# Kernel optimization log

Measured on AMD Instinct MI355X. Metric: run time of the kernel, lower is better.

The kernel has to match this reference:

```python
import jax, jax.numpy as jnp
import numpy as np

F_IN, N_TREES, DEPTH, TREE_DIM, BATCH = 256, 512, 6, 3, 512


def entmax15_axis0(z):
    """Exact 1.5-entmax along axis 0 (sort-based algorithm from Peters et al. 2019)."""
    z = z / 2.0
    z = z - jnp.max(z, axis=0, keepdims=True)
    zs = -jnp.sort(-z, axis=0)                      # descending sort, [F, N]
    F = z.shape[0]
    rho = jnp.arange(1, F + 1, dtype=z.dtype)[:, None]
    mean = jnp.cumsum(zs, axis=0) / rho
    mean_sq = jnp.cumsum(zs * zs, axis=0) / rho
    ss = rho * (mean_sq - mean * mean)
    delta = (1.0 - ss) / rho
    tau = mean - jnp.sqrt(jnp.clip(delta, 0.0))
    support = (tau <= zs).astype(jnp.int32)
    k = jnp.sum(support, axis=0) - 1                # last valid index per column
    tau_star = jnp.take_along_axis(tau, k[None, :], axis=0)
    return jnp.square(jnp.clip(z - tau_star, 0.0))


def setup_inputs() -> dict:
    key = jax.random.key(0)
    k0, k1, k2, k3 = jax.random.split(key, 4)
    return {
        "input": jax.random.normal(k0, (BATCH, F_IN), jnp.float32),
        "feat_attention": jax.random.uniform(k1, (F_IN, N_TREES * DEPTH), jnp.float32),
        "feature_thresholds": jax.random.normal(k2, (N_TREES, DEPTH), jnp.float32) * 0.1,
        "log_temperatures": jnp.zeros((N_TREES, DEPTH), jnp.float32),
        "response": jax.random.normal(k3, (N_TREES, TREE_DIM, 2 ** DEPTH), jnp.float32),
    }


def reference(input, feat_attention, feature_thresholds, log_temperatures, response):
    T, D = feature_thresholds.shape
    F = feat_attention.shape[0]
    # sparse feature selection per (tree, depth)
    choice_weight = entmax15_axis0(feat_attention).reshape(F, T, D)
    feature_values = jnp.einsum('bi,ind->bnd', input, choice_weight)      # [B, T, D]
    # thresholding with learned temperature, bin_func == '05_01'
    tl = (feature_values - feature_thresholds) * jnp.exp(-log_temperatures)
    tl = jnp.stack([-tl, tl], axis=-1)                                    # [B, T, D, 2]
    bins = jnp.clip(0.5 * tl + 0.5, -0.5, 1.5)
    # binary codes of the 2^D leaves: [D, 2^D, 2]
    idx = jnp.arange(2 ** D)
    off = 2 ** jnp.arange(D)
    bc = ((idx[None, :] // off[:, None]) % 2).astype(bins.dtype)
    codes = jnp.stack([bc, 1.0 - bc], axis=-1)
    # depth-wise outer product into leaf weights
    bin_matches = jnp.einsum('btds,dcs->btdc', bins, codes)               # [B, T, D, 2^D]
    response_weights = jnp.prod(bin_matches, axis=-2)                     # [B, T, 2^D]
    out = jnp.einsum('bnd,ncd->bnc', response_weights, response)          # [B, T, C]
    return out.reshape(out.shape[0], -1)
```

## Files before the change

### kernel.cpp

```cpp
#include <hip/hip_runtime.h>
#include <math.h>

#define F_IN 256
#define NTREES 512
#define DEPTH 6
#define NCOLS (NTREES * DEPTH)
#define BATCH 512
#define OUTW (NTREES * 3)

__global__ __launch_bounds__(256) void k_entmax(const float* __restrict__ att,
                                                float* __restrict__ cw) {
    const int n0 = blockIdx.x * 16;
    const int tid = threadIdx.x;
    const int lane = tid & 63;
    const int w = tid >> 6;
    __shared__ float s_z[16][260];

    const int cld = tid & 15;
#pragma unroll
    for (int it = 0; it < 16; ++it) {
        int f = (tid >> 4) + it * 16;
        s_z[cld][f] = att[f * NCOLS + n0 + cld];
    }
    __syncthreads();

    float4 z[4];
    float m[4], tau[4];
#pragma unroll
    for (int c = 0; c < 4; ++c) {
        float4 v = *(const float4*)&s_z[w * 4 + c][4 * lane];
        z[c] = make_float4(v.x * 0.5f, v.y * 0.5f, v.z * 0.5f, v.w * 0.5f);
        m[c] = fmaxf(fmaxf(z[c].x, z[c].y), fmaxf(z[c].z, z[c].w));
    }
#pragma unroll
    for (int off = 32; off >= 1; off >>= 1)
#pragma unroll
        for (int c = 0; c < 4; ++c)
            m[c] = fmaxf(m[c], __shfl_xor(m[c], off));
#pragma unroll
    for (int c = 0; c < 4; ++c) {
        z[c].x -= m[c]; z[c].y -= m[c]; z[c].z -= m[c]; z[c].w -= m[c];
        tau[c] = -1.0f;
    }

    for (int iter = 0; iter < 14; ++iter) {
        float S1[4], S2[4];
#pragma unroll
        for (int c = 0; c < 4; ++c) {
            float d0 = fmaxf(z[c].x - tau[c], 0.f);
            float d1 = fmaxf(z[c].y - tau[c], 0.f);
            float d2 = fmaxf(z[c].z - tau[c], 0.f);
            float d3 = fmaxf(z[c].w - tau[c], 0.f);
            S1[c] = (d0 + d1) + (d2 + d3);
            S2[c] = fmaf(d0, d0, fmaf(d1, d1, fmaf(d2, d2, d3 * d3)));
        }
#pragma unroll
        for (int off = 32; off >= 1; off >>= 1)
#pragma unroll
            for (int c = 0; c < 4; ++c) {
                S1[c] += __shfl_xor(S1[c], off);
                S2[c] += __shfl_xor(S2[c], off);
            }
        bool done = true;
#pragma unroll
        for (int c = 0; c < 4; ++c) {
            tau[c] += (S2[c] - 1.f) / (2.f * S1[c]);
            done = done && (fabsf(S2[c] - 1.f) < 4e-6f);
        }
        if (done) break;
    }

#pragma unroll
    for (int c = 0; c < 4; ++c) {
        float4 pv;
        float v0 = fmaxf(z[c].x - tau[c], 0.f);
        float v1 = fmaxf(z[c].y - tau[c], 0.f);
        float v2 = fmaxf(z[c].z - tau[c], 0.f);
        float v3 = fmaxf(z[c].w - tau[c], 0.f);
        pv.x = v0 * v0; pv.y = v1 * v1; pv.z = v2 * v2; pv.w = v3 * v3;
        *(float4*)&s_z[w * 4 + c][4 * lane] = pv;
    }
    __syncthreads();
#pragma unroll
    for (int it = 0; it < 16; ++it) {
        int f = (tid >> 4) + it * 16;
        cw[f * NCOLS + n0 + cld] = s_z[cld][f];
    }
}

__global__ __launch_bounds__(256) void k_gemm(const float* __restrict__ cw,
                                              const float* __restrict__ inp,
                                              float* __restrict__ fv) {
    const int n0 = blockIdx.x * 64;
    const int b0 = blockIdx.y * 64;
    const int tid = threadIdx.x;
    __shared__ float sA[16][64];
    __shared__ float sB[16][68];
    const int tx = tid & 15, ty = tid >> 4;
    const int a_k = tid >> 4, a_n = (tid & 15) * 4;
    const int b_b = tid >> 2, b_k = (tid & 3) * 4;
    float acc[4][4] = {};
    for (int f0 = 0; f0 < F_IN; f0 += 16) {
        float4 av = *(const float4*)&cw[(f0 + a_k) * NCOLS + n0 + a_n];
        float4 bv = *(const float4*)&inp[(b0 + b_b) * F_IN + f0 + b_k];
        __syncthreads();
        *(float4*)&sA[a_k][a_n] = av;
        sB[b_k + 0][b_b] = bv.x;
        sB[b_k + 1][b_b] = bv.y;
        sB[b_k + 2][b_b] = bv.z;
        sB[b_k + 3][b_b] = bv.w;
        __syncthreads();
#pragma unroll
        for (int kk = 0; kk < 16; ++kk) {
            float a[4], b[4];
#pragma unroll
            for (int i = 0; i < 4; ++i) a[i] = sA[kk][ty * 4 + i];
#pragma unroll
            for (int j = 0; j < 4; ++j) b[j] = sB[kk][tx * 4 + j];
#pragma unroll
            for (int i = 0; i < 4; ++i)
#pragma unroll
                for (int j = 0; j < 4; ++j)
                    acc[i][j] = fmaf(a[i], b[j], acc[i][j]);
        }
    }
#pragma unroll
    for (int i = 0; i < 4; ++i) {
        float4 v = make_float4(acc[i][0], acc[i][1], acc[i][2], acc[i][3]);
        *(float4*)&fv[(n0 + ty * 4 + i) * BATCH + b0 + tx * 4] = v;
    }
}

__global__ __launch_bounds__(256) void k_tree(const float* __restrict__ fv,
                                              const float* __restrict__ thr,
                                              const float* __restrict__ ltemp,
                                              const float* __restrict__ resp,
                                              float* __restrict__ out) {
    const int t0 = blockIdx.x * 8;
    const int b0 = blockIdx.y * 64;
    const int tid = threadIdx.x;
    const int bl = tid & 63;
    const int b = b0 + bl;
    const int tsub = tid >> 6;
    __shared__ float s_resp[8 * 192];
    __shared__ float s_out[64][25];

    for (int i = tid; i < 8 * 192; i += 256)
        s_resp[i] = resp[t0 * 192 + i];
    __syncthreads();

#pragma unroll
    for (int half_t = 0; half_t < 2; ++half_t) {
        const int ttl = tsub + half_t * 4;
        const int tt = t0 + ttl;
        float bpos[6], bneg[6];
#pragma unroll
        for (int d = 0; d < 6; ++d) {
            float fvv = fv[(tt * 6 + d) * BATCH + b];
            float tl = (fvv - thr[tt * 6 + d]) * expf(-ltemp[tt * 6 + d]);
            float hp = 0.5f * tl + 0.5f;
            float hn = 0.5f - 0.5f * tl;
            bpos[d] = fminf(fmaxf(hp, -0.5f), 1.5f);
            bneg[d] = fminf(fmaxf(hn, -0.5f), 1.5f);
        }
        float p[64];
        p[0] = 1.f;
#pragma unroll
        for (int d = 0; d < 6; ++d) {
            int half = 1 << d;
#pragma unroll 32
            for (int i = half - 1; i >= 0; --i) {
                float v = p[i];
                p[i + half] = v * bneg[d];
                p[i]        = v * bpos[d];
            }
        }
        float a0 = 0.f, a1 = 0.f, a2 = 0.f;
        const float* r = &s_resp[ttl * 192];
#pragma unroll
        for (int c = 0; c < 64; ++c) {
            a0 = fmaf(p[c], r[c], a0);
            a1 = fmaf(p[c], r[64 + c], a1);
            a2 = fmaf(p[c], r[128 + c], a2);
        }
        s_out[bl][ttl * 3 + 0] = a0;
        s_out[bl][ttl * 3 + 1] = a1;
        s_out[bl][ttl * 3 + 2] = a2;
    }
    __syncthreads();
    for (int i = tid; i < 64 * 24; i += 256) {
        int row = i / 24, col = i % 24;
        out[(b0 + row) * OUTW + t0 * 3 + col] = s_out[row][col];
    }
}

extern "C" void kernel_launch(void* const* d_in, const int* in_sizes, int n_in,
                              void* d_out, int out_size, void* d_ws, size_t ws_size,
                              hipStream_t stream) {
    const float* input = (const float*)d_in[0];
    const float* att   = (const float*)d_in[1];
    const float* thr   = (const float*)d_in[2];
    const float* ltemp = (const float*)d_in[3];
    const float* resp  = (const float*)d_in[4];
    float* out = (float*)d_out;

    float* cw = (float*)d_ws;
    float* fv = cw + F_IN * NCOLS;

    hipLaunchKernelGGL(k_entmax, dim3(NCOLS / 16), dim3(256), 0, stream, att, cw);
    hipLaunchKernelGGL(k_gemm, dim3(NCOLS / 64, BATCH / 64), dim3(256), 0, stream,
                       cw, input, fv);
    hipLaunchKernelGGL(k_tree, dim3(NTREES / 8, BATCH / 64), dim3(256), 0, stream,
                       fv, thr, ltemp, resp, out);
}
```

Baseline: 98.39 us.

## Fuse feature GEMM with tree evaluation and store choice weights transposed

The GEMM and tree-evaluation kernels become one kernel. Each block computes the 48 feature values for its 8 trees and 64 batch rows into shared memory, then evaluates the trees directly, so the fv intermediate no longer makes a round trip through global memory and one launch is dropped. The entmax kernel now writes the choice weights transposed (column-major over features) with float4 stores, and the GEMM uses a K-tile of 64 with a 3x4 register tile. The trade-offs are higher shared-memory use per block (about 47KB), which may lower occupancy, and a smaller per-thread register tile in the GEMM.

```diff
diff --git a/kernel.cpp b/kernel.cpp
--- a/kernel.cpp
+++ b/kernel.cpp
@@ -9,7 +9,7 @@
 #define OUTW (NTREES * 3)
 
 __global__ __launch_bounds__(256) void k_entmax(const float* __restrict__ att,
-                                                float* __restrict__ cw) {
+                                                float* __restrict__ cwT) {
     const int n0 = blockIdx.x * 16;
     const int tid = threadIdx.x;
     const int lane = tid & 63;
@@ -81,116 +81,134 @@
         *(float4*)&s_z[w * 4 + c][4 * lane] = pv;
     }
     __syncthreads();
-#pragma unroll
-    for (int it = 0; it < 16; ++it) {
-        int f = (tid >> 4) + it * 16;
-        cw[f * NCOLS + n0 + cld] = s_z[cld][f];
+    const int nl = tid >> 4;
+    const int f0 = (tid & 15) * 16;
+#pragma unroll
+    for (int j = 0; j < 4; ++j) {
+        float4 v = *(const float4*)&s_z[nl][f0 + 4 * j];
+        *(float4*)&cwT[(n0 + nl) * F_IN + f0 + 4 * j] = v;
     }
 }
 
-__global__ __launch_bounds__(256) void k_gemm(const float* __restrict__ cw,
-                                              const float* __restrict__ inp,
-                                              float* __restrict__ fv) {
-    const int n0 = blockIdx.x * 64;
-    const int b0 = blockIdx.y * 64;
+__global__ __launch_bounds__(256) void k_fused(const float* __restrict__ cwT,
+                                               const float* __restrict__ inp,
+                                               const float* __restrict__ thr,
+                                               const float* __restrict__ ltemp,
+                                               const float* __restrict__ resp,
+                                               float* __restrict__ out) {
+    const int tb  = blockIdx.x;
+    const int b0  = blockIdx.y * 64;
+    const int t0g = tb * 8;
+    const int n0g = tb * 48;
     const int tid = threadIdx.x;
-    __shared__ float sA[16][64];
-    __shared__ float sB[16][68];
-    const int tx = tid & 15, ty = tid >> 4;
-    const int a_k = tid >> 4, a_n = (tid & 15) * 4;
-    const int b_b = tid >> 2, b_k = (tid & 3) * 4;
-    float acc[4][4] = {};
-    for (int f0 = 0; f0 < F_IN; f0 += 16) {
-        float4 av = *(const float4*)&cw[(f0 + a_k) * NCOLS + n0 + a_n];
-        float4 bv = *(const float4*)&inp[(b0 + b_b) * F_IN + f0 + b_k];
+
+    __shared__ float sA[64][48];
+    __shared__ float sB[64][68];
+    __shared__ float sFV[48][68];
+    __shared__ float sR[8 * 192];
+    __shared__ float sO[64][25];
+
+    for (int i = tid; i < 8 * 192; i += 256) sR[i] = resp[t0g * 192 + i];
+
+    const int tx = tid & 15;
+    const int ty = tid >> 4;
+    const int a_w = tid >> 6;
+    const int a_k = tid & 63;
+    const int b_b = tid >> 2;
+    const int b_k = (tid & 3) * 16;
+    float acc[3][4] = {};
+
+    for (int k0 = 0; k0 < F_IN; k0 += 64) {
+        float a_reg[12];
+#pragma unroll
+        for (int i = 0; i < 12; ++i)
+            a_reg[i] = cwT[(n0g + i * 4 + a_w) * F_IN + k0 + a_k];
+        float4 b_reg[4];
+#pragma unroll
+        for (int i = 0; i < 4; ++i)
+            b_reg[i] = *(const float4*)&inp[(b0 + b_b) * F_IN + k0 + b_k + i * 4];
         __syncthreads();
-        *(float4*)&sA[a_k][a_n] = av;
-        sB[b_k + 0][b_b] = bv.x;
-        sB[b_k + 1][b_b] = bv.y;
-        sB[b_k + 2][b_b] = bv.z;
-        sB[b_k + 3][b_b] = bv.w;
+#pragma unroll
+        for (int i = 0; i < 12; ++i) sA[a_k][i * 4 + a_w] = a_reg[i];
+#pragma unroll
+        for (int i = 0; i < 4; ++i) {
+            sB[b_k + i * 4 + 0][b_b] = b_reg[i].x;
+            sB[b_k + i * 4 + 1][b_b] = b_reg[i].y;
+            sB[b_k + i * 4 + 2][b_b] = b_reg[i].z;
+            sB[b_k + i * 4 + 3][b_b] = b_reg[i].w;
+        }
         __syncthreads();
-#pragma unroll
-        for (int kk = 0; kk < 16; ++kk) {
-            float a[4], b[4];
-#pragma unroll
-            for (int i = 0; i < 4; ++i) a[i] = sA[kk][ty * 4 + i];
-#pragma unroll
-            for (int j = 0; j < 4; ++j) b[j] = sB[kk][tx * 4 + j];
-#pragma unroll
-            for (int i = 0; i < 4; ++i)
-#pragma unroll
-                for (int j = 0; j < 4; ++j)
-                    acc[i][j] = fmaf(a[i], b[j], acc[i][j]);
-        }
-    }
-#pragma unroll
-    for (int i = 0; i < 4; ++i) {
-        float4 v = make_float4(acc[i][0], acc[i][1], acc[i][2], acc[i][3]);
-        *(float4*)&fv[(n0 + ty * 4 + i) * BATCH + b0 + tx * 4] = v;
-    }
-}
-
-__global__ __launch_bounds__(256) void k_tree(const float* __restrict__ fv,
-                                              const float* __restrict__ thr,
-                                              const float* __restrict__ ltemp,
-                                              const float* __restrict__ resp,
-                                              float* __restrict__ out) {
-    const int t0 = blockIdx.x * 8;
-    const int b0 = blockIdx.y * 64;
-    const int tid = threadIdx.x;
-    const int bl = tid & 63;
-    const int b = b0 + bl;
-    const int tsub = tid >> 6;
-    __shared__ float s_resp[8 * 192];
-    __shared__ float s_out[64][25];
-
-    for (int i = tid; i < 8 * 192; i += 256)
-        s_resp[i] = resp[t0 * 192 + i];
-    __syncthreads();
-
-#pragma unroll
-    for (int half_t = 0; half_t < 2; ++half_t) {
-        const int ttl = tsub + half_t * 4;
-        const int tt = t0 + ttl;
+#pragma unroll 16
+        for (int kk = 0; kk < 64; ++kk) {
+            float a0 = sA[kk][ty * 3 + 0];
+            float a1 = sA[kk][ty * 3 + 1];
+            float a2 = sA[kk][ty * 3 + 2];
+            float4 bv = *(const float4*)&sB[kk][tx * 4];
+            acc[0][0] = fmaf(a0, bv.x, acc[0][0]);
+            acc[0][1] = fmaf(a0, bv.y, acc[0][1]);
+            acc[0][2] = fmaf(a0, bv.z, acc[0][2]);
+            acc[0][3] = fmaf(a0, bv.w, acc[0][3]);
+            acc[1][0] = fmaf(a1, bv.x, acc[1][0]);
+            acc[1][1] = fmaf(a1, bv.y, acc[1][1]);
+            acc[1][2] = fmaf(a1, bv.z, acc[1][2]);
+            acc[1][3] = fmaf(a1, bv.w, acc[1][3]);
+            acc[2][0] = fmaf(a2, bv.x, acc[2][0]);
+            acc[2][1] = fmaf(a2, bv.y, acc[2][1]);
+            acc[2][2] = fmaf(a2, bv.z, acc[2][2]);
+            acc[2][3] = fmaf(a2, bv.w, acc[2][3]);
+        }
+    }
+#pragma unroll
+    for (int r = 0; r < 3; ++r) {
+        float4 v = make_float4(acc[r][0], acc[r][1], acc[r][2], acc[r][3]);
+        *(float4*)&sFV[ty * 3 + r][tx * 4] = v;
+    }
+    __syncthreads();
+
+#pragma unroll
+    for (int p = 0; p < 2; ++p) {
+        const int pi = p * 256 + tid;
+        const int tl = pi >> 6;
+        const int b  = pi & 63;
+        const int base = (t0g + tl) * 6;
         float bpos[6], bneg[6];
 #pragma unroll
         for (int d = 0; d < 6; ++d) {
-            float fvv = fv[(tt * 6 + d) * BATCH + b];
-            float tl = (fvv - thr[tt * 6 + d]) * expf(-ltemp[tt * 6 + d]);
-            float hp = 0.5f * tl + 0.5f;
-            float hn = 0.5f - 0.5f * tl;
+            float fvv = sFV[tl * 6 + d][b];
+            float tlv = (fvv - thr[base + d]) * expf(-ltemp[base + d]);
+            float hp = 0.5f * tlv + 0.5f;
+            float hn = 0.5f - 0.5f * tlv;
             bpos[d] = fminf(fmaxf(hp, -0.5f), 1.5f);
             bneg[d] = fminf(fmaxf(hn, -0.5f), 1.5f);
         }
-        float p[64];
-        p[0] = 1.f;
+        float pr[64];
+        pr[0] = 1.f;
 #pragma unroll
         for (int d = 0; d < 6; ++d) {
             int half = 1 << d;
 #pragma unroll 32
             for (int i = half - 1; i >= 0; --i) {
-                float v = p[i];
-                p[i + half] = v * bneg[d];
-                p[i]        = v * bpos[d];
+                float v = pr[i];
+                pr[i + half] = v * bneg[d];
+                pr[i]        = v * bpos[d];
             }
         }
         float a0 = 0.f, a1 = 0.f, a2 = 0.f;
-        const float* r = &s_resp[ttl * 192];
+        const float* r = &sR[tl * 192];
 #pragma unroll
         for (int c = 0; c < 64; ++c) {
-            a0 = fmaf(p[c], r[c], a0);
-            a1 = fmaf(p[c], r[64 + c], a1);
-            a2 = fmaf(p[c], r[128 + c], a2);
-        }
-        s_out[bl][ttl * 3 + 0] = a0;
-        s_out[bl][ttl * 3 + 1] = a1;
-        s_out[bl][ttl * 3 + 2] = a2;
+            a0 = fmaf(pr[c], r[c], a0);
+            a1 = fmaf(pr[c], r[64 + c], a1);
+            a2 = fmaf(pr[c], r[128 + c], a2);
+        }
+        sO[b][tl * 3 + 0] = a0;
+        sO[b][tl * 3 + 1] = a1;
+        sO[b][tl * 3 + 2] = a2;
     }
     __syncthreads();
     for (int i = tid; i < 64 * 24; i += 256) {
         int row = i / 24, col = i % 24;
-        out[(b0 + row) * OUTW + t0 * 3 + col] = s_out[row][col];
+        out[(b0 + row) * OUTW + t0g * 3 + col] = sO[row][col];
     }
 }
 
@@ -204,12 +222,9 @@
     const float* resp  = (const float*)d_in[4];
     float* out = (float*)d_out;
 
-    float* cw = (float*)d_ws;
-    float* fv = cw + F_IN * NCOLS;
-
-    hipLaunchKernelGGL(k_entmax, dim3(NCOLS / 16), dim3(256), 0, stream, att, cw);
-    hipLaunchKernelGGL(k_gemm, dim3(NCOLS / 64, BATCH / 64), dim3(256), 0, stream,
-                       cw, input, fv);
-    hipLaunchKernelGGL(k_tree, dim3(NTREES / 8, BATCH / 64), dim3(256), 0, stream,
-                       fv, thr, ltemp, resp, out);
+    float* cwT = (float*)d_ws;
+
+    hipLaunchKernelGGL(k_entmax, dim3(NCOLS / 16), dim3(256), 0, stream, att, cwT);
+    hipLaunchKernelGGL(k_fused, dim3(NTREES / 8, BATCH / 64), dim3(256), 0, stream,
+                       cwT, input, thr, ltemp, resp, out);
 }
```

Result: slower. 101.3 us (+2.9%).

## Run feature GEMM on bf16 MFMA with hi/lo split for fp32 accuracy

Applied to the files above, without the earlier changes.

The fp32 SIMT GEMM is replaced by a matrix-core kernel that uses bf16 16x16x32 MFMA. Each operand is split into bf16 high and low parts, and three products (hh, hl, lh) are accumulated to approximate fp32 precision. The entmax kernel now writes the choice weights transposed and pre-split. Extra blocks in the same launch split the input matrix, so the GEMM reads K-contiguous operands straight from global memory with no LDS. The cost is three times the MFMA work and extra workspace traffic for the split arrays, plus a small accuracy risk from the dropped lo*lo term.

```diff
diff --git a/kernel.cpp b/kernel.cpp
--- a/kernel.cpp
+++ b/kernel.cpp
@@ -8,10 +8,48 @@
 #define BATCH 512
 #define OUTW (NTREES * 3)
 
+typedef __attribute__((ext_vector_type(8))) short bf16x8;
+typedef __attribute__((ext_vector_type(4))) float f32x4;
+typedef __attribute__((ext_vector_type(4))) unsigned short u16x4;
+typedef __attribute__((ext_vector_type(8))) unsigned short u16x8;
+
+__device__ __forceinline__ unsigned short f2bf(float x) {
+    unsigned u = __float_as_uint(x);
+    return (unsigned short)((u + 0x7FFFu + ((u >> 16) & 1u)) >> 16);
+}
+__device__ __forceinline__ void split2(float x, unsigned short& h, unsigned short& l) {
+    h = f2bf(x);
+    l = f2bf(x - __uint_as_float((unsigned)h << 16));
+}
+
 __global__ __launch_bounds__(256) void k_entmax(const float* __restrict__ att,
-                                                float* __restrict__ cw) {
+                                                const float* __restrict__ inp,
+                                                unsigned short* __restrict__ cwT_hi,
+                                                unsigned short* __restrict__ cwT_lo,
+                                                unsigned short* __restrict__ in_hi,
+                                                unsigned short* __restrict__ in_lo) {
+    const int tid = threadIdx.x;
+
+    if (blockIdx.x >= NCOLS / 16) {
+        const int cb = blockIdx.x - NCOLS / 16;
+        const float4* src = (const float4*)inp;
+#pragma unroll
+        for (int it = 0; it < 16; ++it) {
+            int idx = cb * 4096 + it * 256 + tid;
+            float4 v = src[idx];
+            u16x4 h, l;
+            unsigned short th, tl;
+            split2(v.x, th, tl); h.x = th; l.x = tl;
+            split2(v.y, th, tl); h.y = th; l.y = tl;
+            split2(v.z, th, tl); h.z = th; l.z = tl;
+            split2(v.w, th, tl); h.w = th; l.w = tl;
+            *(u16x4*)&in_hi[idx * 4] = h;
+            *(u16x4*)&in_lo[idx * 4] = l;
+        }
+        return;
+    }
+
     const int n0 = blockIdx.x * 16;
-    const int tid = threadIdx.x;
     const int lane = tid & 63;
     const int w = tid >> 6;
     __shared__ float s_z[16][260];
@@ -81,54 +119,75 @@
         *(float4*)&s_z[w * 4 + c][4 * lane] = pv;
     }
     __syncthreads();
-#pragma unroll
-    for (int it = 0; it < 16; ++it) {
-        int f = (tid >> 4) + it * 16;
-        cw[f * NCOLS + n0 + cld] = s_z[cld][f];
-    }
-}
-
-__global__ __launch_bounds__(256) void k_gemm(const float* __restrict__ cw,
-                                              const float* __restrict__ inp,
+    const int nl = tid >> 4;
+    const int f0 = (tid & 15) * 16;
+#pragma unroll
+    for (int j = 0; j < 2; ++j) {
+        u16x8 hv, lv;
+#pragma unroll
+        for (int e = 0; e < 8; ++e) {
+            unsigned short h, l;
+            split2(s_z[nl][f0 + j * 8 + e], h, l);
+            hv[e] = h; lv[e] = l;
+        }
+        *(u16x8*)&cwT_hi[(n0 + nl) * F_IN + f0 + j * 8] = hv;
+        *(u16x8*)&cwT_lo[(n0 + nl) * F_IN + f0 + j * 8] = lv;
+    }
+}
+
+__global__ __launch_bounds__(128) void k_gemm(const unsigned short* __restrict__ Ah,
+                                              const unsigned short* __restrict__ Al,
+                                              const unsigned short* __restrict__ Bh,
+                                              const unsigned short* __restrict__ Bl,
                                               float* __restrict__ fv) {
-    const int n0 = blockIdx.x * 64;
-    const int b0 = blockIdx.y * 64;
     const int tid = threadIdx.x;
-    __shared__ float sA[16][64];
-    __shared__ float sB[16][68];
-    const int tx = tid & 15, ty = tid >> 4;
-    const int a_k = tid >> 4, a_n = (tid & 15) * 4;
-    const int b_b = tid >> 2, b_k = (tid & 3) * 4;
-    float acc[4][4] = {};
-    for (int f0 = 0; f0 < F_IN; f0 += 16) {
-        float4 av = *(const float4*)&cw[(f0 + a_k) * NCOLS + n0 + a_n];
-        float4 bv = *(const float4*)&inp[(b0 + b_b) * F_IN + f0 + b_k];
-        __syncthreads();
-        *(float4*)&sA[a_k][a_n] = av;
-        sB[b_k + 0][b_b] = bv.x;
-        sB[b_k + 1][b_b] = bv.y;
-        sB[b_k + 2][b_b] = bv.z;
-        sB[b_k + 3][b_b] = bv.w;
-        __syncthreads();
-#pragma unroll
-        for (int kk = 0; kk < 16; ++kk) {
-            float a[4], b[4];
-#pragma unroll
-            for (int i = 0; i < 4; ++i) a[i] = sA[kk][ty * 4 + i];
-#pragma unroll
-            for (int j = 0; j < 4; ++j) b[j] = sB[kk][tx * 4 + j];
-#pragma unroll
-            for (int i = 0; i < 4; ++i)
-#pragma unroll
-                for (int j = 0; j < 4; ++j)
-                    acc[i][j] = fmaf(a[i], b[j], acc[i][j]);
-        }
-    }
-#pragma unroll
-    for (int i = 0; i < 4; ++i) {
-        float4 v = make_float4(acc[i][0], acc[i][1], acc[i][2], acc[i][3]);
-        *(float4*)&fv[(n0 + ty * 4 + i) * BATCH + b0 + tx * 4] = v;
-    }
+    const int wave = tid >> 6, lane = tid & 63;
+    const int quad = lane >> 4, lr = lane & 15;
+    const int n0 = blockIdx.x * 32;
+    const int bw = blockIdx.y * 128 + wave * 64;
+
+    const unsigned short* pah = Ah + (n0 + lr) * F_IN + quad * 8;
+    const unsigned short* pal = Al + (n0 + lr) * F_IN + quad * 8;
+    const unsigned short* pbh = Bh + (bw + lr) * F_IN + quad * 8;
+    const unsigned short* pbl = Bl + (bw + lr) * F_IN + quad * 8;
+
+    f32x4 acc[2][4];
+#pragma unroll
+    for (int i = 0; i < 2; ++i)
+#pragma unroll
+        for (int j = 0; j < 4; ++j)
+            acc[i][j] = (f32x4){0.f, 0.f, 0.f, 0.f};
+
+#pragma unroll
+    for (int k0 = 0; k0 < F_IN; k0 += 32) {
+        bf16x8 ah[2], al[2], bh[4], bl[4];
+#pragma unroll
+        for (int i = 0; i < 2; ++i) {
+            ah[i] = *(const bf16x8*)(pah + i * 16 * F_IN + k0);
+            al[i] = *(const bf16x8*)(pal + i * 16 * F_IN + k0);
+        }
+#pragma unroll
+        for (int j = 0; j < 4; ++j) {
+            bh[j] = *(const bf16x8*)(pbh + j * 16 * F_IN + k0);
+            bl[j] = *(const bf16x8*)(pbl + j * 16 * F_IN + k0);
+        }
+#pragma unroll
+        for (int i = 0; i < 2; ++i)
+#pragma unroll
+            for (int j = 0; j < 4; ++j) {
+                acc[i][j] = __builtin_amdgcn_mfma_f32_16x16x32_bf16(ah[i], bh[j], acc[i][j], 0, 0, 0);
+                acc[i][j] = __builtin_amdgcn_mfma_f32_16x16x32_bf16(ah[i], bl[j], acc[i][j], 0, 0, 0);
+                acc[i][j] = __builtin_amdgcn_mfma_f32_16x16x32_bf16(al[i], bh[j], acc[i][j], 0, 0, 0);
+            }
+    }
+
+#pragma unroll
+    for (int i = 0; i < 2; ++i)
+#pragma unroll
+        for (int j = 0; j < 4; ++j)
+#pragma unroll
+            for (int r = 0; r < 4; ++r)
+                fv[(n0 + 16 * i + quad * 4 + r) * BATCH + bw + 16 * j + lr] = acc[i][j][r];
 }
 
 __global__ __launch_bounds__(256) void k_tree(const float* __restrict__ fv,
@@ -204,12 +263,16 @@
     const float* resp  = (const float*)d_in[4];
     float* out = (float*)d_out;
 
-    float* cw = (float*)d_ws;
-    float* fv = cw + F_IN * NCOLS;
-
-    hipLaunchKernelGGL(k_entmax, dim3(NCOLS / 16), dim3(256), 0, stream, att, cw);
-    hipLaunchKernelGGL(k_gemm, dim3(NCOLS / 64, BATCH / 64), dim3(256), 0, stream,
-                       cw, input, fv);
+    unsigned short* cwT_hi = (unsigned short*)d_ws;
+    unsigned short* cwT_lo = cwT_hi + NCOLS * F_IN;
+    unsigned short* in_hi  = cwT_lo + NCOLS * F_IN;
+    unsigned short* in_lo  = in_hi + BATCH * F_IN;
+    float* fv = (float*)(in_lo + BATCH * F_IN);
+
+    hipLaunchKernelGGL(k_entmax, dim3(NCOLS / 16 + 8), dim3(256), 0, stream,
+                       att, input, cwT_hi, cwT_lo, in_hi, in_lo);
+    hipLaunchKernelGGL(k_gemm, dim3(NCOLS / 32, BATCH / 128), dim3(128), 0, stream,
+                       cwT_hi, cwT_lo, in_hi, in_lo, fv);
     hipLaunchKernelGGL(k_tree, dim3(NTREES / 8, BATCH / 64), dim3(256), 0, stream,
                        fv, thr, ltemp, resp, out);
 }
```

Measured after the change: 95.69 us. 2.7% less time.
